# Optimization experiments

Measured on AMD Instinct MI355X. Metric: run time of the kernel, lower is better.

Reference implementation:

```python
import jax, jax.numpy as jnp
import numpy as np
from functools import partial

D, T, I, H, W = 90, 96, 512, 1024, 64


def setup_inputs() -> dict:
    key = jax.random.key(0)
    ks = jax.random.split(key, 32)
    stdv = 1.0 / np.sqrt(H)
    u = lambda k, shape: jax.random.uniform(k, shape, jnp.float32, -stdv, stdv)
    inp = {
        "x_input": jax.random.normal(ks[0], (D, T, I), jnp.float32),
        "x_weather": jax.random.normal(ks[1], (D, T, W), jnp.float32),
        "w_ix": u(ks[2], (H, I)), "w_ih": u(ks[3], (H, H)), "w_ie": u(ks[4], (H, H)), "b_i": u(ks[5], (H,)),
        "w_fx": u(ks[6], (H, I)), "w_fo": u(ks[7], (H, H)), "w_fe": u(ks[8], (H, H)), "b_f": u(ks[9], (H,)),
        "w_ox": u(ks[10], (H, I)), "w_oh": u(ks[11], (H, H)), "w_oe": u(ks[12], (H, H)), "b_o": u(ks[13], (H,)),
        "w_gx": u(ks[14], (H, I)), "w_gh": u(ks[15], (H, H)), "b_g": u(ks[16], (H,)),
        "w_d": u(ks[17], (H, I)), "w_w": u(ks[18], (H, I)), "w_m": u(ks[19], (H, I)),
        "w_t": u(ks[20], (H, H)), "w_e": u(ks[21], (H, W)), "b_e": u(ks[22], (H,)),
    }
    return inp


def reference(x_input, x_weather,
              w_ix, w_ih, w_ie, b_i,
              w_fx, w_fo, w_fe, b_f,
              w_ox, w_oh, w_oe, b_o,
              w_gx, w_gh, b_g,
              w_d, w_w, w_m, w_t, w_e, b_e):
    d_size, t_size, _ = x_input.shape
    h_size = w_ix.shape[0]
    d_idx = jnp.arange(d_size)

    def day_shift(shift, min_d):
        # x_input[d - shift] when d >= min_d else 0; % replicates torch negative-index wrap
        src = x_input[(d_idx - shift) % d_size]           # [D,T,I]
        return jnp.where((d_idx >= min_d)[:, None, None], src, 0.0)

    h_d = day_shift(1, 1)     # previous day
    h_w = day_shift(6, 7)     # "week" lookback (d-6, as in original)
    h_m = day_shift(29, 28)   # "month" lookback (d-29, as in original)

    mm = lambda a, w: jnp.einsum('dtf,hf->dth', a, w)
    pre_ho = mm(h_d, w_d) + mm(h_w, w_w) + mm(h_m, w_m)                    # [D,T,H]
    e = jax.nn.sigmoid(mm(x_weather, w_e) + b_e)                           # [D,T,H]
    pre_i = mm(x_input, w_ix) + jnp.einsum('dth,gh->dtg', e, w_ie) + b_i
    pre_g = mm(x_input, w_gx) + b_g
    pre_f = mm(x_input, w_fx) + jnp.einsum('dth,gh->dtg', e, w_fe) + b_f
    pre_o = mm(x_input, w_ox) + jnp.einsum('dth,gh->dtg', e, w_oe) + b_o

    n = d_size * t_size
    flat = lambda a: a.reshape(n, h_size)
    xs = (flat(pre_ho), flat(pre_i), flat(pre_g), flat(pre_f), flat(pre_o))

    def step(carry, inp):
        h_t, c_t = carry
        ph, pi, pg, pf, po = inp
        h_o = jax.nn.sigmoid(ph + 2.0 * (w_t @ h_t))   # original adds w_t@h_t twice
        i = jax.nn.sigmoid(pi + w_ih @ h_o)
        g = jnp.tanh(pg + w_gh @ h_o)
        f = jax.nn.sigmoid(pf + w_fo @ h_o)
        o = jax.nn.sigmoid(po + w_oh @ h_t)
        c = f * c_t + i * g
        h = o * jnp.tanh(c)
        return (h, c), (h, c)

    init = (jnp.zeros((h_size,), x_input.dtype), jnp.zeros((h_size,), x_input.dtype))
    _, (hs, cs) = jax.lax.scan(step, init, xs)
    return hs.reshape(d_size, t_size, h_size), cs.reshape(d_size, t_size, h_size)
```

## Files before the change

### kernel.cpp

```cpp
#include <hip/hip_runtime.h>
#include <cstdio>

#define NROWS 8640
#define HDIM  1024
#define NWG   64
#define RPW   16
#define LINE_W 32

typedef float vf4 __attribute__((ext_vector_type(4)));

__device__ __forceinline__ float fsig(float x)  { return 1.f / (1.f + __expf(-x)); }
__device__ __forceinline__ float ftanh(float x) { return 2.f / (1.f + __expf(-2.f * x)) - 1.f; }

__device__ __forceinline__ vf4 llc_load_f4(const float* p) {
  vf4 v;
  asm volatile("global_load_dwordx4 %0, %1, off sc0 sc1\n\ts_waitcnt vmcnt(0)"
               : "=v"(v) : "v"(p) : "memory");
  return v;
}
__device__ __forceinline__ void llc_store_f4(float* p, vf4 v) {
  asm volatile("global_store_dwordx4 %0, %1, off sc0 sc1" :: "v"(p), "v"(v) : "memory");
}

__device__ __forceinline__ float dot4(vf4 a, vf4 b) {
  return a.x*b.x + a.y*b.y + a.z*b.z + a.w*b.w;
}

#define WRED(x) { x += __shfl_xor(x,32,64); x += __shfl_xor(x,16,64); \
                  x += __shfl_xor(x, 8,64); x += __shfl_xor(x, 4,64); \
                  x += __shfl_xor(x, 2,64); x += __shfl_xor(x, 1,64); }

__global__ __launch_bounds__(512, 2) void scan_kernel(
    const float* __restrict__ pre_ho, const float* __restrict__ pre_i,
    const float* __restrict__ pre_g,  const float* __restrict__ pre_f,
    const float* __restrict__ pre_o,
    const float* __restrict__ w_t,  const float* __restrict__ w_ih,
    const float* __restrict__ w_gh, const float* __restrict__ w_fo,
    const float* __restrict__ w_oh,
    float* __restrict__ lines0, float* __restrict__ lines1,
    float* __restrict__ hs, float* __restrict__ cs)
{
  __shared__ float h_sh[HDIM];

  const int tid  = threadIdx.x;
  const int lane = tid & 63;
  const int w    = tid >> 6;
  const int wg   = blockIdx.x;
  const int r0   = wg * RPW + 2 * w;
  const int myrow = r0 + lane;

  for (int i = tid; i < HDIM; i += 512) h_sh[i] = 0.f;

  vf4 Wf[5][2][4];
  {
    const float* Wp[5] = { w_t, w_oh, w_ih, w_gh, w_fo };
#pragma unroll
    for (int mt = 0; mt < 5; ++mt)
#pragma unroll
      for (int rr = 0; rr < 2; ++rr)
#pragma unroll
        for (int m = 0; m < 4; ++m)
          Wf[mt][rr][m] = *(const vf4*)(Wp[mt] + (long)(r0+rr)*HDIM + m*256 + 4*lane);
  }

  float cprev = 0.f, oo = 0.f;
  float ph = 0.f, po = 0.f, pi = 0.f, pg = 0.f, pf = 0.f;
  if (lane < 2) {
    ph = pre_ho[myrow]; po = pre_o[myrow];
    pi = pre_i[myrow];  pg = pre_g[myrow]; pf = pre_f[myrow];
  }

  const long pofs = (long)(tid >> 3) * LINE_W + (long)(tid & 7) * 4;
  const int  dsh  = 2 * tid;
  const float* pollA = lines0 + pofs;
  const float* pollB = lines1 + pofs;
  float* pubA = lines0 + (long)wg * LINE_W + (long)w * 4;
  float* pubB = lines1 + (long)wg * LINE_W + (long)w * 4;

  __syncthreads();

  for (int n = 0; n < NROWS; ++n) {
    const int tgtA = 2*n + 1, tgtB = 2*n + 2;

    {
      vf4 h0 = *(const vf4*)(h_sh + 4*lane);
      vf4 h1 = *(const vf4*)(h_sh + 4*lane + 256);
      vf4 h2 = *(const vf4*)(h_sh + 4*lane + 512);
      vf4 h3 = *(const vf4*)(h_sh + 4*lane + 768);
      float t0 = dot4(Wf[0][0][0],h0)+dot4(Wf[0][0][1],h1)+dot4(Wf[0][0][2],h2)+dot4(Wf[0][0][3],h3);
      float t1 = dot4(Wf[0][1][0],h0)+dot4(Wf[0][1][1],h1)+dot4(Wf[0][1][2],h2)+dot4(Wf[0][1][3],h3);
      float o0 = dot4(Wf[1][0][0],h0)+dot4(Wf[1][0][1],h1)+dot4(Wf[1][0][2],h2)+dot4(Wf[1][0][3],h3);
      float o1 = dot4(Wf[1][1][0],h0)+dot4(Wf[1][1][1],h1)+dot4(Wf[1][1][2],h2)+dot4(Wf[1][1][3],h3);
      WRED(t0); WRED(t1); WRED(o0); WRED(o1);
      float hov = 0.f;
      if (lane < 2) {
        float ut = lane ? t1 : t0;
        float uo = lane ? o1 : o0;
        hov = fsig(ph + 2.f * ut);
        oo  = fsig(po + uo);
      }
      float hon = __shfl_xor(hov, 1, 64);
      if (lane == 0) {
        vf4 d; d.x = hov; d.y = hon; d.z = __int_as_float(tgtA); d.w = 0.f;
        llc_store_f4(pubA, d);
      }
    }
    __syncthreads();
    {
      vf4 d;
      do { d = llc_load_f4(pollA); } while (__float_as_int(d.z) < tgtA);
      *(float2*)(h_sh + dsh) = make_float2(d.x, d.y);
    }
    __syncthreads();

    {
      float ph2 = 0.f, po2 = 0.f, pi2 = 0.f, pg2 = 0.f, pf2 = 0.f;
      if (lane < 2 && n + 1 < NROWS) {
        long o2 = (long)(n+1)*HDIM + myrow;
        ph2 = pre_ho[o2]; po2 = pre_o[o2];
        pi2 = pre_i[o2];  pg2 = pre_g[o2]; pf2 = pre_f[o2];
      }
      vf4 h0 = *(const vf4*)(h_sh + 4*lane);
      vf4 h1 = *(const vf4*)(h_sh + 4*lane + 256);
      vf4 h2 = *(const vf4*)(h_sh + 4*lane + 512);
      vf4 h3 = *(const vf4*)(h_sh + 4*lane + 768);
      float i0 = dot4(Wf[2][0][0],h0)+dot4(Wf[2][0][1],h1)+dot4(Wf[2][0][2],h2)+dot4(Wf[2][0][3],h3);
      float i1 = dot4(Wf[2][1][0],h0)+dot4(Wf[2][1][1],h1)+dot4(Wf[2][1][2],h2)+dot4(Wf[2][1][3],h3);
      float g0 = dot4(Wf[3][0][0],h0)+dot4(Wf[3][0][1],h1)+dot4(Wf[3][0][2],h2)+dot4(Wf[3][0][3],h3);
      float g1 = dot4(Wf[3][1][0],h0)+dot4(Wf[3][1][1],h1)+dot4(Wf[3][1][2],h2)+dot4(Wf[3][1][3],h3);
      float f0 = dot4(Wf[4][0][0],h0)+dot4(Wf[4][0][1],h1)+dot4(Wf[4][0][2],h2)+dot4(Wf[4][0][3],h3);
      float f1 = dot4(Wf[4][1][0],h0)+dot4(Wf[4][1][1],h1)+dot4(Wf[4][1][2],h2)+dot4(Wf[4][1][3],h3);
      WRED(i0); WRED(i1); WRED(g0); WRED(g1); WRED(f0); WRED(f1);
      float hhv = 0.f;
      if (lane < 2) {
        float ui = lane ? i1 : i0;
        float ug = lane ? g1 : g0;
        float uf = lane ? f1 : f0;
        float ii = fsig(pi + ui);
        float gg = ftanh(pg + ug);
        float ff = fsig(pf + uf);
        float cc = ff * cprev + ii * gg;
        hhv = oo * ftanh(cc);
        cprev = cc;
        hs[(long)n*HDIM + myrow] = hhv;
        cs[(long)n*HDIM + myrow] = cc;
      }
      float hhn = __shfl_xor(hhv, 1, 64);
      if (lane == 0) {
        vf4 d; d.x = hhv; d.y = hhn; d.z = __int_as_float(tgtB); d.w = 0.f;
        llc_store_f4(pubB, d);
      }
      ph = ph2; po = po2; pi = pi2; pg = pg2; pf = pf2;
    }
    __syncthreads();
    {
      vf4 d;
      do { d = llc_load_f4(pollB); } while (__float_as_int(d.z) < tgtB);
      *(float2*)(h_sh + dsh) = make_float2(d.x, d.y);
    }
    __syncthreads();
  }
}

__global__ __launch_bounds__(256) void gemm_acc(
    float* __restrict__ C, const float* __restrict__ A, const float* __restrict__ B,
    int K, int shift, int minn)
{
  __shared__ float Asf[16 * 68];
  __shared__ float Bsf[16 * 68];
  const int tid = threadIdx.x;
  const int h0  = blockIdx.x * 64;
  const int n0  = blockIdx.y * 64;
  const int r   = tid >> 2;
  const int kq  = (tid & 3) << 2;
  const int tx  = tid & 15, ty = tid >> 4;

  int arow = n0 + r;
  int src  = arow - shift; if (src < 0) src += NROWS;
  const bool avalid = (arow >= minn);
  const float* Ap = A + (long)src * K + kq;
  const float* Bp = B + (long)(h0 + r) * K + kq;

  vf4 acc0 = {0.f,0.f,0.f,0.f}, acc1 = {0.f,0.f,0.f,0.f};
  vf4 acc2 = {0.f,0.f,0.f,0.f}, acc3 = {0.f,0.f,0.f,0.f};
  const vf4 zero = {0.f,0.f,0.f,0.f};

  for (int k0 = 0; k0 < K; k0 += 16) {
    vf4 av = avalid ? *(const vf4*)(Ap + k0) : zero;
    vf4 bv = *(const vf4*)(Bp + k0);
    __syncthreads();
    Asf[(kq+0)*68 + r] = av.x;  Asf[(kq+1)*68 + r] = av.y;
    Asf[(kq+2)*68 + r] = av.z;  Asf[(kq+3)*68 + r] = av.w;
    Bsf[(kq+0)*68 + r] = bv.x;  Bsf[(kq+1)*68 + r] = bv.y;
    Bsf[(kq+2)*68 + r] = bv.z;  Bsf[(kq+3)*68 + r] = bv.w;
    __syncthreads();
#pragma unroll
    for (int c = 0; c < 16; ++c) {
      vf4 a = *(const vf4*)(Asf + c*68 + (ty << 2));
      vf4 b = *(const vf4*)(Bsf + c*68 + (tx << 2));
      acc0 += a.x * b;
      acc1 += a.y * b;
      acc2 += a.z * b;
      acc3 += a.w * b;
    }
  }
  float* cp = C + (long)(n0 + (ty << 2)) * HDIM + h0 + (tx << 2);
  { vf4 t = *(vf4*)(cp + 0*HDIM); t += acc0; *(vf4*)(cp + 0*HDIM) = t; }
  { vf4 t = *(vf4*)(cp + 1*HDIM); t += acc1; *(vf4*)(cp + 1*HDIM) = t; }
  { vf4 t = *(vf4*)(cp + 2*HDIM); t += acc2; *(vf4*)(cp + 2*HDIM) = t; }
  { vf4 t = *(vf4*)(cp + 3*HDIM); t += acc3; *(vf4*)(cp + 3*HDIM) = t; }
}

__global__ void bias_init(float* __restrict__ out, const float* __restrict__ bias) {
  int i = blockIdx.x * blockDim.x + threadIdx.x;
  vf4 v = {0.f,0.f,0.f,0.f};
  if (bias) { int h = (i << 2) & (HDIM - 1); v = *(const vf4*)(bias + h); }
  *((vf4*)out + i) = v;
}

__global__ void sigmoid_k(float* __restrict__ e) {
  int i = blockIdx.x * blockDim.x + threadIdx.x;
  vf4 v = *((vf4*)e + i);
  v.x = fsig(v.x); v.y = fsig(v.y); v.z = fsig(v.z); v.w = fsig(v.w);
  *((vf4*)e + i) = v;
}

extern "C" void kernel_launch(void* const* d_in, const int* in_sizes, int n_in,
                              void* d_out, int out_size, void* d_ws, size_t ws_size,
                              hipStream_t stream) {
  const float* x    = (const float*)d_in[0];
  const float* xw   = (const float*)d_in[1];
  const float* w_ix = (const float*)d_in[2];
  const float* w_ih = (const float*)d_in[3];
  const float* w_ie = (const float*)d_in[4];
  const float* b_i  = (const float*)d_in[5];
  const float* w_fx = (const float*)d_in[6];
  const float* w_fo = (const float*)d_in[7];
  const float* w_fe = (const float*)d_in[8];
  const float* b_f  = (const float*)d_in[9];
  const float* w_ox = (const float*)d_in[10];
  const float* w_oh = (const float*)d_in[11];
  const float* w_oe = (const float*)d_in[12];
  const float* b_o  = (const float*)d_in[13];
  const float* w_gx = (const float*)d_in[14];
  const float* w_gh = (const float*)d_in[15];
  const float* b_g  = (const float*)d_in[16];
  const float* w_d  = (const float*)d_in[17];
  const float* w_w  = (const float*)d_in[18];
  const float* w_m  = (const float*)d_in[19];
  const float* w_t  = (const float*)d_in[20];
  const float* w_e  = (const float*)d_in[21];
  const float* b_e  = (const float*)d_in[22];

  const long S = (long)NROWS * HDIM;
  float* ws_f   = (float*)d_ws;
  float* pre_ho = ws_f + 0*S;
  float* pre_i  = ws_f + 1*S;
  float* pre_g  = ws_f + 2*S;
  float* pre_f  = ws_f + 3*S;
  float* pre_o  = ws_f + 4*S;
  float* e_buf  = ws_f + 5*S;
  float* lines0 = ws_f + 6*S;
  float* lines1 = lines0 + NWG*LINE_W;

  size_t need = (size_t)(6*S + 2*NWG*LINE_W) * sizeof(float);
  if (ws_size < need) {
    fprintf(stderr, "kernel_launch: ws too small (have %zu, need %zu)\n", ws_size, need);
    return;
  }

  dim3 ggrid(HDIM/64, NROWS/64);

  bias_init<<<NROWS, 256, 0, stream>>>(pre_i, b_i);
  bias_init<<<NROWS, 256, 0, stream>>>(pre_g, b_g);
  bias_init<<<NROWS, 256, 0, stream>>>(pre_f, b_f);
  bias_init<<<NROWS, 256, 0, stream>>>(pre_o, b_o);
  bias_init<<<NROWS, 256, 0, stream>>>(e_buf, b_e);
  bias_init<<<NROWS, 256, 0, stream>>>(pre_ho, nullptr);

  gemm_acc<<<ggrid, 256, 0, stream>>>(e_buf, xw, w_e, 64, 0, 0);
  sigmoid_k<<<NROWS, 256, 0, stream>>>(e_buf);

  gemm_acc<<<ggrid, 256, 0, stream>>>(pre_i, x, w_ix, 512, 0, 0);
  gemm_acc<<<ggrid, 256, 0, stream>>>(pre_g, x, w_gx, 512, 0, 0);
  gemm_acc<<<ggrid, 256, 0, stream>>>(pre_f, x, w_fx, 512, 0, 0);
  gemm_acc<<<ggrid, 256, 0, stream>>>(pre_o, x, w_ox, 512, 0, 0);
  gemm_acc<<<ggrid, 256, 0, stream>>>(pre_i, e_buf, w_ie, 1024, 0, 0);
  gemm_acc<<<ggrid, 256, 0, stream>>>(pre_f, e_buf, w_fe, 1024, 0, 0);
  gemm_acc<<<ggrid, 256, 0, stream>>>(pre_o, e_buf, w_oe, 1024, 0, 0);
  gemm_acc<<<ggrid, 256, 0, stream>>>(pre_ho, x, w_d, 512,   96,   96);
  gemm_acc<<<ggrid, 256, 0, stream>>>(pre_ho, x, w_w, 512,  576,  672);
  gemm_acc<<<ggrid, 256, 0, stream>>>(pre_ho, x, w_m, 512, 2784, 2688);

  hipMemsetAsync(lines0, 0, 2 * NWG * LINE_W * sizeof(float), stream);

  float* hs = (float*)d_out;
  float* cs = hs + S;
  scan_kernel<<<NWG, 512, 0, stream>>>(pre_ho, pre_i, pre_g, pre_f, pre_o,
                                       w_t, w_ih, w_gh, w_fo, w_oh,
                                       lines0, lines1, hs, cs);
}
```

Baseline: 46.66 ms.

## Replicate publish lines 8x and double-buffer shared h to drop barriers

Each wave now writes its published pair of hidden values to 8 replicas of the exchange buffer, and each workgroup polls the replica selected by its index. This spreads polling traffic from 64 workgroups over more cache lines to reduce contention. Shared memory is split into two buffers (one for h_o, one for h), so the barrier before polling in each half-step can be removed. This saves two workgroup barriers per time step, at the cost of 8x more publish stores and a larger exchange buffer.

```diff
diff --git a/kernel.cpp b/kernel.cpp
--- a/kernel.cpp
+++ b/kernel.cpp
@@ -6,6 +6,8 @@
 #define NWG   64
 #define RPW   16
 #define LINE_W 32
+#define NREP  8
+#define REPSTR (NWG * LINE_W)
 
 typedef float vf4 __attribute__((ext_vector_type(4)));
 
@@ -40,7 +42,8 @@
     float* __restrict__ lines0, float* __restrict__ lines1,
     float* __restrict__ hs, float* __restrict__ cs)
 {
-  __shared__ float h_sh[HDIM];
+  __shared__ float sh_a[HDIM];
+  __shared__ float sh_b[HDIM];
 
   const int tid  = threadIdx.x;
   const int lane = tid & 63;
@@ -49,7 +52,7 @@
   const int r0   = wg * RPW + 2 * w;
   const int myrow = r0 + lane;
 
-  for (int i = tid; i < HDIM; i += 512) h_sh[i] = 0.f;
+  for (int i = tid; i < HDIM; i += 512) { sh_a[i] = 0.f; sh_b[i] = 0.f; }
 
   vf4 Wf[5][2][4];
   {
@@ -70,12 +73,13 @@
     pi = pre_i[myrow];  pg = pre_g[myrow]; pf = pre_f[myrow];
   }
 
-  const long pofs = (long)(tid >> 3) * LINE_W + (long)(tid & 7) * 4;
+  const long pofs = (long)(wg & 7) * REPSTR + (long)(tid >> 3) * LINE_W + (long)(tid & 7) * 4;
   const int  dsh  = 2 * tid;
   const float* pollA = lines0 + pofs;
   const float* pollB = lines1 + pofs;
-  float* pubA = lines0 + (long)wg * LINE_W + (long)w * 4;
-  float* pubB = lines1 + (long)wg * LINE_W + (long)w * 4;
+  const long pubofs = (long)lane * REPSTR + (long)wg * LINE_W + (long)w * 4;
+  float* pubA = lines0 + pubofs;
+  float* pubB = lines1 + pubofs;
 
   __syncthreads();
 
@@ -83,10 +87,10 @@
     const int tgtA = 2*n + 1, tgtB = 2*n + 2;
 
     {
-      vf4 h0 = *(const vf4*)(h_sh + 4*lane);
-      vf4 h1 = *(const vf4*)(h_sh + 4*lane + 256);
-      vf4 h2 = *(const vf4*)(h_sh + 4*lane + 512);
-      vf4 h3 = *(const vf4*)(h_sh + 4*lane + 768);
+      vf4 h0 = *(const vf4*)(sh_a + 4*lane);
+      vf4 h1 = *(const vf4*)(sh_a + 4*lane + 256);
+      vf4 h2 = *(const vf4*)(sh_a + 4*lane + 512);
+      vf4 h3 = *(const vf4*)(sh_a + 4*lane + 768);
       float t0 = dot4(Wf[0][0][0],h0)+dot4(Wf[0][0][1],h1)+dot4(Wf[0][0][2],h2)+dot4(Wf[0][0][3],h3);
       float t1 = dot4(Wf[0][1][0],h0)+dot4(Wf[0][1][1],h1)+dot4(Wf[0][1][2],h2)+dot4(Wf[0][1][3],h3);
       float o0 = dot4(Wf[1][0][0],h0)+dot4(Wf[1][0][1],h1)+dot4(Wf[1][0][2],h2)+dot4(Wf[1][0][3],h3);
@@ -99,17 +103,17 @@
         hov = fsig(ph + 2.f * ut);
         oo  = fsig(po + uo);
       }
-      float hon = __shfl_xor(hov, 1, 64);
-      if (lane == 0) {
-        vf4 d; d.x = hov; d.y = hon; d.z = __int_as_float(tgtA); d.w = 0.f;
+      float d0 = __shfl(hov, 0, 64);
+      float d1 = __shfl(hov, 1, 64);
+      if (lane < NREP) {
+        vf4 d; d.x = d0; d.y = d1; d.z = __int_as_float(tgtA); d.w = 0.f;
         llc_store_f4(pubA, d);
       }
     }
-    __syncthreads();
     {
       vf4 d;
       do { d = llc_load_f4(pollA); } while (__float_as_int(d.z) < tgtA);
-      *(float2*)(h_sh + dsh) = make_float2(d.x, d.y);
+      *(float2*)(sh_b + dsh) = make_float2(d.x, d.y);
     }
     __syncthreads();
 
@@ -120,10 +124,10 @@
         ph2 = pre_ho[o2]; po2 = pre_o[o2];
         pi2 = pre_i[o2];  pg2 = pre_g[o2]; pf2 = pre_f[o2];
       }
-      vf4 h0 = *(const vf4*)(h_sh + 4*lane);
-      vf4 h1 = *(const vf4*)(h_sh + 4*lane + 256);
-      vf4 h2 = *(const vf4*)(h_sh + 4*lane + 512);
-      vf4 h3 = *(const vf4*)(h_sh + 4*lane + 768);
+      vf4 h0 = *(const vf4*)(sh_b + 4*lane);
+      vf4 h1 = *(const vf4*)(sh_b + 4*lane + 256);
+      vf4 h2 = *(const vf4*)(sh_b + 4*lane + 512);
+      vf4 h3 = *(const vf4*)(sh_b + 4*lane + 768);
       float i0 = dot4(Wf[2][0][0],h0)+dot4(Wf[2][0][1],h1)+dot4(Wf[2][0][2],h2)+dot4(Wf[2][0][3],h3);
       float i1 = dot4(Wf[2][1][0],h0)+dot4(Wf[2][1][1],h1)+dot4(Wf[2][1][2],h2)+dot4(Wf[2][1][3],h3);
       float g0 = dot4(Wf[3][0][0],h0)+dot4(Wf[3][0][1],h1)+dot4(Wf[3][0][2],h2)+dot4(Wf[3][0][3],h3);
@@ -145,18 +149,18 @@
         hs[(long)n*HDIM + myrow] = hhv;
         cs[(long)n*HDIM + myrow] = cc;
       }
-      float hhn = __shfl_xor(hhv, 1, 64);
-      if (lane == 0) {
-        vf4 d; d.x = hhv; d.y = hhn; d.z = __int_as_float(tgtB); d.w = 0.f;
+      float d0 = __shfl(hhv, 0, 64);
+      float d1 = __shfl(hhv, 1, 64);
+      if (lane < NREP) {
+        vf4 d; d.x = d0; d.y = d1; d.z = __int_as_float(tgtB); d.w = 0.f;
         llc_store_f4(pubB, d);
       }
       ph = ph2; po = po2; pi = pi2; pg = pg2; pf = pf2;
     }
-    __syncthreads();
     {
       vf4 d;
       do { d = llc_load_f4(pollB); } while (__float_as_int(d.z) < tgtB);
-      *(float2*)(h_sh + dsh) = make_float2(d.x, d.y);
+      *(float2*)(sh_a + dsh) = make_float2(d.x, d.y);
     }
     __syncthreads();
   }
@@ -261,9 +265,9 @@
   float* pre_o  = ws_f + 4*S;
   float* e_buf  = ws_f + 5*S;
   float* lines0 = ws_f + 6*S;
-  float* lines1 = lines0 + NWG*LINE_W;
-
-  size_t need = (size_t)(6*S + 2*NWG*LINE_W) * sizeof(float);
+  float* lines1 = lines0 + NREP*REPSTR;
+
+  size_t need = (size_t)(6*S + 2*NREP*REPSTR) * sizeof(float);
   if (ws_size < need) {
     fprintf(stderr, "kernel_launch: ws too small (have %zu, need %zu)\n", ws_size, need);
     return;
@@ -292,7 +296,7 @@
   gemm_acc<<<ggrid, 256, 0, stream>>>(pre_ho, x, w_w, 512,  576,  672);
   gemm_acc<<<ggrid, 256, 0, stream>>>(pre_ho, x, w_m, 512, 2784, 2688);
 
-  hipMemsetAsync(lines0, 0, 2 * NWG * LINE_W * sizeof(float), stream);
+  hipMemsetAsync(lines0, 0, 2 * NREP * REPSTR * sizeof(float), stream);
 
   float* hs = (float*)d_out;
   float* cs = hs + S;
```

After: 58.42 ms. 1.25x slower.
